# Kernel optimization log

Hardware: AMD Instinct MI355X
Metric: run time of the kernel (lower is better)

Reference implementation:

```python
import jax, jax.numpy as jnp
import numpy as np

H = 512  # hidden_size

def setup_inputs() -> dict:
    key = jax.random.key(0)
    ks = jax.random.split(key, 5)
    B, S = 2, 512
    feats = jax.random.normal(ks[0], (B, S, H), dtype=jnp.float32)
    # torch Linear init ~ U(-1/sqrt(in), 1/sqrt(in)); scaled normals are fine for a reference
    W1 = jax.random.normal(ks[1], (2 * H, H), dtype=jnp.float32) / np.sqrt(2 * H)
    b1 = jnp.zeros((H,), dtype=jnp.float32)
    W2 = jax.random.normal(ks[2], (H, H // 2), dtype=jnp.float32) / np.sqrt(H)
    b2 = jnp.zeros((H // 2,), dtype=jnp.float32)
    W3 = jax.random.normal(ks[3], (H // 2, 1), dtype=jnp.float32) / np.sqrt(H // 2)
    b3 = jnp.zeros((1,), dtype=jnp.float32)
    return {"features": feats, "W1": W1, "b1": b1, "W2": W2, "b2": b2, "W3": W3, "b3": b3}


def reference(features, W1, b1, W2, b2, W3, b3):
    # cat([f_i, f_j]) @ W1 == f_i @ W1[:H] + f_j @ W1[H:]
    # Precompute the two halves once per residue instead of per pair.
    a = jnp.einsum('bsh,hk->bsk', features, W1[:H])          # [B,S,H]
    c = jnp.einsum('bsh,hk->bsk', features, W1[H:])          # [B,S,H]
    h1 = jax.nn.relu(a[:, :, None, :] + c[:, None, :, :] + b1)  # [B,S,S,H]
    # Dropout(0.1) is identity at inference.
    h2 = jax.nn.relu(jnp.einsum('bijh,hk->bijk', h1, W2) + b2)  # [B,S,S,H//2]
    logits = jnp.einsum('bijk,ko->bijo', h2, W3) + b3            # [B,S,S,1]
    return jax.nn.sigmoid(logits[..., 0])                        # [B,S,S]
```

## Files before the change

kernel.cpp:

```cpp
#include <hip/hip_runtime.h>

#define S_DIM 512
#define H_DIM 512
#define NH 256
#define TI 8
#define TJ 8

#define AS1 __attribute__((address_space(1)))
#define AS3 __attribute__((address_space(3)))

typedef _Float16 half8 __attribute__((ext_vector_type(8)));
typedef _Float16 half4 __attribute__((ext_vector_type(4)));
typedef float f32x4 __attribute__((ext_vector_type(4)));

__global__ __launch_bounds__(256) void convert_feats_kernel(const float* __restrict__ f,
                                                            _Float16* __restrict__ o) {
    int t = blockIdx.x * 256 + threadIdx.x;
    float4 v = ((const float4*)f)[t];
    half4 h;
    h.x = (_Float16)v.x; h.y = (_Float16)v.y; h.z = (_Float16)v.z; h.w = (_Float16)v.w;
    ((half4*)o)[t] = h;
}

__global__ __launch_bounds__(256) void convert_w1_kernel(const float* __restrict__ W1,
                                                         _Float16* __restrict__ w1L) {
    int t = blockIdx.x * 256 + threadIdx.x;
    int gcb = t >> 10, n = t & 1023;
    const float* src = (n < H_DIM) ? &W1[(size_t)(gcb * 8) * H_DIM + n]
                                   : &W1[(size_t)(H_DIM + gcb * 8) * H_DIM + (n - H_DIM)];
    half8 v;
#pragma unroll
    for (int j = 0; j < 8; j++) v[j] = (_Float16)src[(size_t)j * H_DIM];
    *(half8*)&w1L[((size_t)gcb * 1024 + n) * 8] = v;
}

__global__ __launch_bounds__(256) void convert_w2_kernel(const float* __restrict__ W2,
                                                         _Float16* __restrict__ w2L) {
    int t = blockIdx.x * 256 + threadIdx.x;
    int gcb = t >> 8, n = t & 255;
    half8 v;
#pragma unroll
    for (int j = 0; j < 8; j++) v[j] = (_Float16)W2[(size_t)(gcb * 8 + j) * NH + n];
    *(half8*)&w2L[((size_t)gcb * 256 + n) * 8] = v;
}

__global__ __launch_bounds__(256) void prep_mfma_kernel(const _Float16* __restrict__ f16,
        const _Float16* __restrict__ w1L, const float* __restrict__ b1,
        _Float16* __restrict__ aH, _Float16* __restrict__ cH) {
    const int n0 = blockIdx.x * 64, m0 = blockIdx.y * 64;
    const int tid = threadIdx.x, wave = tid >> 6, lane = tid & 63;
    const int quad = lane >> 4, l16 = lane & 15;
    const int wm = wave >> 1, wn = wave & 1;
    int mrow[2], ncol[2];
#pragma unroll
    for (int mt = 0; mt < 2; mt++) mrow[mt] = m0 + wm * 32 + mt * 16 + l16;
#pragma unroll
    for (int nt = 0; nt < 2; nt++) ncol[nt] = n0 + wn * 32 + nt * 16 + l16;
    f32x4 acc[2][2];
#pragma unroll
    for (int mt = 0; mt < 2; mt++)
#pragma unroll
        for (int nt = 0; nt < 2; nt++) acc[mt][nt] = (f32x4)0.f;
#pragma unroll
    for (int ks = 0; ks < 16; ks++) {
        int gcb = ks * 4 + quad;
        half8 af[2], bf[2];
#pragma unroll
        for (int mt = 0; mt < 2; mt++)
            af[mt] = *(const half8*)&f16[(size_t)mrow[mt] * H_DIM + gcb * 8];
#pragma unroll
        for (int nt = 0; nt < 2; nt++)
            bf[nt] = *(const half8*)&w1L[((size_t)gcb * 1024 + ncol[nt]) * 8];
#pragma unroll
        for (int nt = 0; nt < 2; nt++)
#pragma unroll
            for (int mt = 0; mt < 2; mt++)
                acc[mt][nt] = __builtin_amdgcn_mfma_f32_16x16x32_f16(af[mt], bf[nt],
                                                                     acc[mt][nt], 0, 0, 0);
    }
    const bool first_half = (n0 < H_DIM);
#pragma unroll
    for (int nt = 0; nt < 2; nt++) {
        float bias = first_half ? b1[ncol[nt]] : 0.f;
#pragma unroll
        for (int mt = 0; mt < 2; mt++)
#pragma unroll
            for (int r = 0; r < 4; r++) {
                int m = m0 + wm * 32 + mt * 16 + quad * 4 + r;
                float v = acc[mt][nt][r] + bias;
                if (first_half) aH[(size_t)m * H_DIM + ncol[nt]] = (_Float16)v;
                else            cH[(size_t)m * H_DIM + (ncol[nt] - H_DIM)] = (_Float16)v;
            }
    }
}

__global__ __launch_bounds__(256, 3) void pair_kernel(
        const _Float16* __restrict__ aH, const _Float16* __restrict__ cH,
        const _Float16* __restrict__ w2L,
        const float* __restrict__ b2, const float* __restrict__ W3,
        const float* __restrict__ b3, float* __restrict__ out) {
    const int jt = blockIdx.x, it = blockIdx.y, b = blockIdx.z;
    const int i0 = it * TI, j0 = jt * TJ;

    __shared__ __align__(16) _Float16 sa[TI * H_DIM];
    __shared__ __align__(16) _Float16 sc[TJ * H_DIM];
    __shared__ float spart[4][64];

    const int tid = threadIdx.x;
    const int wave = tid >> 6, lane = tid & 63;
    const int quad = lane >> 4, l16 = lane & 15;
    const int wn = wave;
    const int nb = wn * 64;

#pragma unroll
    for (int rr0 = 0; rr0 < 2; rr0++) {
        int rr = rr0 * 4 + wave;
        int gc = (lane & ~7) | ((lane & 7) ^ (rr & 7));
        __builtin_amdgcn_global_load_lds(
            (const AS1 unsigned int*)&aH[((size_t)(b * S_DIM + i0 + rr)) * H_DIM + gc * 8],
            (AS3 unsigned int*)&sa[rr * H_DIM], 16, 0, 0);
        __builtin_amdgcn_global_load_lds(
            (const AS1 unsigned int*)&cH[((size_t)(b * S_DIM + j0 + rr)) * H_DIM + gc * 8],
            (AS3 unsigned int*)&sc[rr * H_DIM], 16, 0, 0);
    }

    int ilrow[4];
#pragma unroll
    for (int mt = 0; mt < 4; mt++) ilrow[mt] = (mt * 16 + l16) >> 3;
    const int jl = l16 & 7;

    f32x4 acc[4][4];
#pragma unroll
    for (int mt = 0; mt < 4; mt++)
#pragma unroll
        for (int nt = 0; nt < 4; nt++) acc[mt][nt] = (f32x4)0.f;

    const _Float16* bbase[4];
#pragma unroll
    for (int nt = 0; nt < 4; nt++) bbase[nt] = &w2L[((size_t)quad * 256 + nb + nt * 16 + l16) * 8];

    half8 bnxt[4];
#pragma unroll
    for (int nt = 0; nt < 4; nt++) bnxt[nt] = *(const half8*)&bbase[nt][0];

    __syncthreads();

#pragma unroll
    for (int ks = 0; ks < 16; ks++) {
        half8 bf[4];
#pragma unroll
        for (int nt = 0; nt < 4; nt++) bf[nt] = bnxt[nt];
        if (ks < 15) {
#pragma unroll
            for (int nt = 0; nt < 4; nt++)
                bnxt[nt] = *(const half8*)&bbase[nt][(size_t)(ks + 1) * 4 * 256 * 8];
        }
        const int gcb = ks * 4 + quad;
        const int slotC = (gcb & ~7) | ((gcb & 7) ^ jl);
        half8 vc = *(const half8*)&sc[jl * H_DIM + slotC * 8];
        half8 af[4];
#pragma unroll
        for (int mt = 0; mt < 4; mt++) {
            int slotA = (gcb & ~7) | ((gcb & 7) ^ (ilrow[mt] & 7));
            half8 va = *(const half8*)&sa[ilrow[mt] * H_DIM + slotA * 8];
            half8 h = va + vc;
#pragma unroll
            for (int e = 0; e < 8; e++)
                h[e] = h[e] > (_Float16)0.f ? h[e] : (_Float16)0.f;
            af[mt] = h;
        }
#pragma unroll
        for (int nt = 0; nt < 4; nt++)
#pragma unroll
            for (int mt = 0; mt < 4; mt++)
                acc[mt][nt] = __builtin_amdgcn_mfma_f32_16x16x32_f16(af[mt], bf[nt],
                                                                     acc[mt][nt], 0, 0, 0);
    }

    float b2v[4], w3v[4];
#pragma unroll
    for (int nt = 0; nt < 4; nt++) {
        int n = nb + nt * 16 + l16;
        b2v[nt] = b2[n];
        w3v[nt] = W3[n];
    }
    float ps[4][4];
#pragma unroll
    for (int mt = 0; mt < 4; mt++)
#pragma unroll
        for (int r = 0; r < 4; r++) {
            float s = 0.f;
#pragma unroll
            for (int nt = 0; nt < 4; nt++) {
                float v = acc[mt][nt][r] + b2v[nt];
                v = v > 0.f ? v : 0.f;
                s += v * w3v[nt];
            }
            ps[mt][r] = s;
        }
#pragma unroll
    for (int mt = 0; mt < 4; mt++)
#pragma unroll
        for (int r = 0; r < 4; r++) {
            float s = ps[mt][r];
            s += __shfl_xor(s, 8, 16);
            s += __shfl_xor(s, 4, 16);
            s += __shfl_xor(s, 2, 16);
            s += __shfl_xor(s, 1, 16);
            ps[mt][r] = s;
        }
    if (l16 == 0) {
#pragma unroll
        for (int mt = 0; mt < 4; mt++)
#pragma unroll
            for (int r = 0; r < 4; r++)
                spart[wn][mt * 16 + quad * 4 + r] = ps[mt][r];
    }
    __syncthreads();
    if (tid < 64) {
        float tot = spart[0][tid] + spart[1][tid] + spart[2][tid] + spart[3][tid] + b3[0];
        float sg = 1.f / (1.f + __expf(-tot));
        int i = i0 + (tid >> 3), j = j0 + (tid & 7);
        out[(size_t)b * S_DIM * S_DIM + (size_t)i * S_DIM + j] = sg;
    }
}

extern "C" void kernel_launch(void* const* d_in, const int* in_sizes, int n_in,
                              void* d_out, int out_size, void* d_ws, size_t ws_size,
                              hipStream_t stream) {
    const float* feats = (const float*)d_in[0];
    const float* W1 = (const float*)d_in[1];
    const float* b1 = (const float*)d_in[2];
    const float* W2 = (const float*)d_in[3];
    const float* b2 = (const float*)d_in[4];
    const float* W3 = (const float*)d_in[5];
    const float* b3 = (const float*)d_in[6];
    float* out = (float*)d_out;

    const int B = in_sizes[0] / (S_DIM * H_DIM);
    const int M = B * S_DIM;

    char* ws = (char*)d_ws;
    _Float16* f16  = (_Float16*)ws;
    _Float16* aH   = (_Float16*)(ws + (1 << 20));
    _Float16* cH   = (_Float16*)(ws + (2 << 20));
    _Float16* w1L  = (_Float16*)(ws + (3 << 20));
    _Float16* w2L  = (_Float16*)(ws + (4 << 20));

    convert_feats_kernel<<<M * H_DIM / 1024, 256, 0, stream>>>(feats, f16);
    convert_w1_kernel<<<256, 256, 0, stream>>>(W1, w1L);
    convert_w2_kernel<<<64, 256, 0, stream>>>(W2, w2L);
    prep_mfma_kernel<<<dim3(16, M / 64), 256, 0, stream>>>(f16, w1L, b1, aH, cH);
    pair_kernel<<<dim3(S_DIM / TJ, S_DIM / TI, B), 256, 0, stream>>>(aH, cH, w2L, b2, W3, b3, out);
}
```

Measured before the change: 229.3 us.

## Fuse conversion kernels, raise pair kernel occupancy, and simplify LDS swizzle

Merges the three fp32-to-fp16 conversion kernels into one launch to cut launch overhead. Raises the pair kernel's launch-bounds occupancy hint from 3 to 4 blocks per CU. Replaces the LDS XOR swizzle with a different permutation and precomputes row offsets so the inner loop needs fewer index operations. Uses a single incremented pointer for the W2 prefetch and a vector max for ReLU. The tighter register budget may cause spills.

After: 209.0 us. 8.9% less time.

```diff
diff --git a/kernel.cpp b/kernel.cpp
--- a/kernel.cpp
+++ b/kernel.cpp
@@ -13,35 +13,35 @@
 typedef _Float16 half4 __attribute__((ext_vector_type(4)));
 typedef float f32x4 __attribute__((ext_vector_type(4)));
 
-__global__ __launch_bounds__(256) void convert_feats_kernel(const float* __restrict__ f,
-                                                            _Float16* __restrict__ o) {
-    int t = blockIdx.x * 256 + threadIdx.x;
-    float4 v = ((const float4*)f)[t];
-    half4 h;
-    h.x = (_Float16)v.x; h.y = (_Float16)v.y; h.z = (_Float16)v.z; h.w = (_Float16)v.w;
-    ((half4*)o)[t] = h;
-}
-
-__global__ __launch_bounds__(256) void convert_w1_kernel(const float* __restrict__ W1,
-                                                         _Float16* __restrict__ w1L) {
-    int t = blockIdx.x * 256 + threadIdx.x;
-    int gcb = t >> 10, n = t & 1023;
-    const float* src = (n < H_DIM) ? &W1[(size_t)(gcb * 8) * H_DIM + n]
-                                   : &W1[(size_t)(H_DIM + gcb * 8) * H_DIM + (n - H_DIM)];
-    half8 v;
-#pragma unroll
-    for (int j = 0; j < 8; j++) v[j] = (_Float16)src[(size_t)j * H_DIM];
-    *(half8*)&w1L[((size_t)gcb * 1024 + n) * 8] = v;
-}
-
-__global__ __launch_bounds__(256) void convert_w2_kernel(const float* __restrict__ W2,
-                                                         _Float16* __restrict__ w2L) {
-    int t = blockIdx.x * 256 + threadIdx.x;
-    int gcb = t >> 8, n = t & 255;
-    half8 v;
-#pragma unroll
-    for (int j = 0; j < 8; j++) v[j] = (_Float16)W2[(size_t)(gcb * 8 + j) * NH + n];
-    *(half8*)&w2L[((size_t)gcb * 256 + n) * 8] = v;
+__device__ __forceinline__ int swz(int r) { return ((r & 1) << 2) | (r >> 1); }
+
+__global__ __launch_bounds__(256) void convert_all_kernel(const float* __restrict__ feats,
+        const float* __restrict__ W1, const float* __restrict__ W2,
+        _Float16* __restrict__ f16, _Float16* __restrict__ w1L, _Float16* __restrict__ w2L) {
+    int blk = blockIdx.x;
+    if (blk < 512) {
+        int t = blk * 256 + threadIdx.x;
+        float4 v = ((const float4*)feats)[t];
+        half4 h;
+        h.x = (_Float16)v.x; h.y = (_Float16)v.y; h.z = (_Float16)v.z; h.w = (_Float16)v.w;
+        ((half4*)f16)[t] = h;
+    } else if (blk < 768) {
+        int t = (blk - 512) * 256 + threadIdx.x;
+        int gcb = t >> 10, n = t & 1023;
+        const float* src = (n < H_DIM) ? &W1[(size_t)(gcb * 8) * H_DIM + n]
+                                       : &W1[(size_t)(H_DIM + gcb * 8) * H_DIM + (n - H_DIM)];
+        half8 v;
+#pragma unroll
+        for (int j = 0; j < 8; j++) v[j] = (_Float16)src[(size_t)j * H_DIM];
+        *(half8*)&w1L[((size_t)gcb * 1024 + n) * 8] = v;
+    } else {
+        int t = (blk - 768) * 256 + threadIdx.x;
+        int gcb = t >> 8, n = t & 255;
+        half8 v;
+#pragma unroll
+        for (int j = 0; j < 8; j++) v[j] = (_Float16)W2[(size_t)(gcb * 8 + j) * NH + n];
+        *(half8*)&w2L[((size_t)gcb * 256 + n) * 8] = v;
+    }
 }
 
 __global__ __launch_bounds__(256) void prep_mfma_kernel(const _Float16* __restrict__ f16,
@@ -94,7 +94,7 @@
     }
 }
 
-__global__ __launch_bounds__(256, 3) void pair_kernel(
+__global__ __launch_bounds__(256, 4) void pair_kernel(
         const _Float16* __restrict__ aH, const _Float16* __restrict__ cH,
         const _Float16* __restrict__ w2L,
         const float* __restrict__ b2, const float* __restrict__ W3,
@@ -115,7 +115,7 @@
 #pragma unroll
     for (int rr0 = 0; rr0 < 2; rr0++) {
         int rr = rr0 * 4 + wave;
-        int gc = (lane & ~7) | ((lane & 7) ^ (rr & 7));
+        int gc = lane ^ swz(rr & 7);
         __builtin_amdgcn_global_load_lds(
             (const AS1 unsigned int*)&aH[((size_t)(b * S_DIM + i0 + rr)) * H_DIM + gc * 8],
             (AS3 unsigned int*)&sa[rr * H_DIM], 16, 0, 0);
@@ -124,10 +124,15 @@
             (AS3 unsigned int*)&sc[rr * H_DIM], 16, 0, 0);
     }
 
-    int ilrow[4];
-#pragma unroll
-    for (int mt = 0; mt < 4; mt++) ilrow[mt] = (mt * 16 + l16) >> 3;
+    int saoff[4], swzA[4];
+#pragma unroll
+    for (int mt = 0; mt < 4; mt++) {
+        int il = (mt * 16 + l16) >> 3;
+        saoff[mt] = il * H_DIM;
+        swzA[mt] = swz(il);
+    }
     const int jl = l16 & 7;
+    const int scoff = jl * H_DIM, swzC = swz(jl);
 
     f32x4 acc[4][4];
 #pragma unroll
@@ -135,13 +140,11 @@
 #pragma unroll
         for (int nt = 0; nt < 4; nt++) acc[mt][nt] = (f32x4)0.f;
 
-    const _Float16* bbase[4];
-#pragma unroll
-    for (int nt = 0; nt < 4; nt++) bbase[nt] = &w2L[((size_t)quad * 256 + nb + nt * 16 + l16) * 8];
+    const _Float16* bp = &w2L[((size_t)quad * 256 + nb + l16) * 8];
 
     half8 bnxt[4];
 #pragma unroll
-    for (int nt = 0; nt < 4; nt++) bnxt[nt] = *(const half8*)&bbase[nt][0];
+    for (int nt = 0; nt < 4; nt++) bnxt[nt] = *(const half8*)&bp[nt * 16 * 8];
 
     __syncthreads();
 
@@ -151,23 +154,18 @@
 #pragma unroll
         for (int nt = 0; nt < 4; nt++) bf[nt] = bnxt[nt];
         if (ks < 15) {
-#pragma unroll
-            for (int nt = 0; nt < 4; nt++)
-                bnxt[nt] = *(const half8*)&bbase[nt][(size_t)(ks + 1) * 4 * 256 * 8];
+            const _Float16* bn = bp + (size_t)4 * 256 * 8;
+#pragma unroll
+            for (int nt = 0; nt < 4; nt++) bnxt[nt] = *(const half8*)&bn[nt * 16 * 8];
+            bp = bn;
         }
         const int gcb = ks * 4 + quad;
-        const int slotC = (gcb & ~7) | ((gcb & 7) ^ jl);
-        half8 vc = *(const half8*)&sc[jl * H_DIM + slotC * 8];
+        half8 vc = *(const half8*)&sc[scoff + (gcb ^ swzC) * 8];
         half8 af[4];
 #pragma unroll
         for (int mt = 0; mt < 4; mt++) {
-            int slotA = (gcb & ~7) | ((gcb & 7) ^ (ilrow[mt] & 7));
-            half8 va = *(const half8*)&sa[ilrow[mt] * H_DIM + slotA * 8];
-            half8 h = va + vc;
-#pragma unroll
-            for (int e = 0; e < 8; e++)
-                h[e] = h[e] > (_Float16)0.f ? h[e] : (_Float16)0.f;
-            af[mt] = h;
+            half8 va = *(const half8*)&sa[saoff[mt] + (gcb ^ swzA[mt]) * 8];
+            af[mt] = __builtin_elementwise_max(va + vc, (half8)(_Float16)0.f);
         }
 #pragma unroll
         for (int nt = 0; nt < 4; nt++)
@@ -247,9 +245,7 @@
     _Float16* w1L  = (_Float16*)(ws + (3 << 20));
     _Float16* w2L  = (_Float16*)(ws + (4 << 20));
 
-    convert_feats_kernel<<<M * H_DIM / 1024, 256, 0, stream>>>(feats, f16);
-    convert_w1_kernel<<<256, 256, 0, stream>>>(W1, w1L);
-    convert_w2_kernel<<<64, 256, 0, stream>>>(W2, w2L);
+    convert_all_kernel<<<832, 256, 0, stream>>>(feats, W1, W2, f16, w1L, w2L);
     prep_mfma_kernel<<<dim3(16, M / 64), 256, 0, stream>>>(f16, w1L, b1, aH, cH);
     pair_kernel<<<dim3(S_DIM / TJ, S_DIM / TI, B), 256, 0, stream>>>(aH, cH, w2L, b2, W3, b3, out);
 }
```
